# Kernel tuning notes

Hardware: AMD Instinct MI355X
Metric: run time of the kernel (lower is better)

Reference implementation:

```python
import jax, jax.numpy as jnp
import numpy as np

N_SEGMENT = 8   # frames per clip (init arg n_segment)
P = 4           # patch_size (init arg)
EPS = 1e-5      # torch F.layer_norm default eps


def setup_inputs() -> dict:
    key = jax.random.key(0)
    # (b*t, c, h, w) = (16*8, 256, 28, 28)
    x = jax.random.normal(key, (128, 256, 28, 28), dtype=jnp.float32)
    return {"x": x}


def _layer_norm(x):
    # F.layer_norm over last dim, no affine params
    m = jnp.mean(x, axis=-1, keepdims=True)
    v = jnp.var(x, axis=-1, keepdims=True)
    return (x - m) * jax.lax.rsqrt(v + EPS)


def _self_attention(x):
    # q = k = v = x; scores = softmax(q k^T / sqrt(E)); out = scores @ v
    e = x.shape[-1]
    scores = jnp.einsum('bqe,bke->bqk', x, x) * (1.0 / float(np.sqrt(e)))
    scores = jax.nn.softmax(scores, axis=-1)
    return jnp.einsum('bqk,bke->bqe', scores, x)


def reference(x):
    t, p = N_SEGMENT, P
    bt, c, h, w = x.shape
    b = bt // t
    ph, pw = h // p, w // p
    e = p * p * c  # patch embedding dim = 4096

    # rearrange '(b t) c (ph p1) (pw p2) -> (b ph pw) t (p1 p2 c)'
    y = x.reshape(b, t, c, ph, p, pw, p)
    y = y.transpose(0, 3, 5, 1, 4, 6, 2).reshape(b * ph * pw, t, e)

    # temporal: layernorm + shift-left-diff + self-attention + residual
    xn = _layer_norm(y)
    xn = jnp.concatenate([xn[:, 1:], jnp.zeros_like(xn[:, :1])], axis=1) - xn
    y = _self_attention(xn) + y

    # rearrange '(b ph pw) t e -> (b t) (ph pw) e'
    y = y.reshape(b, ph, pw, t, e).transpose(0, 3, 1, 2, 4).reshape(b * t, ph * pw, e)

    # spatial: layernorm + self-attention + residual
    xn = _layer_norm(y)
    y = _self_attention(xn) + y

    # rearrange '(b t) (ph pw) (p1 p2 c) -> (b t) c (ph p1) (pw p2)'
    y = y.reshape(b, t, ph, pw, p, p, c)
    y = y.transpose(0, 1, 6, 2, 4, 3, 5).reshape(bt, c, h, w)
    return y
```

## Files before the change

kernel.cpp:

```cpp
#include <hip/hip_runtime.h>


#define IDX36(a,b) ((((a)*8)+(b))-((((a)*((a)+1)))/2))

typedef __attribute__((ext_vector_type(8)))  short bf16x8;
typedef __attribute__((ext_vector_type(16))) float f32x16;

__device__ __forceinline__ float wsum64(float v){
  #pragma unroll
  for (int off=32; off; off>>=1) v += __shfl_xor(v, off);
  return v;
}
__device__ __forceinline__ float wsum32(float v){
  #pragma unroll
  for (int off=16; off; off>>=1) v += __shfl_xor(v, off);
  return v;
}
__device__ __forceinline__ unsigned int rne_bf16(float f){
  unsigned int b = __float_as_uint(f);
  return (b + 0x7FFFu + ((b>>16)&1u)) >> 16;
}

__global__ __launch_bounds__(256) void k_t1(const float* __restrict__ x, float* __restrict__ wsG){
  const int bx = blockIdx.x;
  const int b = bx / 112;
  const int ph = (bx % 112) / 16;
  const int slice = bx & 15;
  const int c0 = slice * 16;
  const int tid = threadIdx.x;

  __shared__ float lds[8*16*116];
  const float4* x4 = reinterpret_cast<const float4*>(x);

  #pragma unroll
  for (int t=0;t<8;t++){
    const int base = ((b*8+t)*256 + c0)*196 + ph*28;
    {
      const int f = tid, c = f/28, m = f%28;
      *reinterpret_cast<float4*>(&lds[(t*16+c)*116 + m*4]) = x4[base + c*196 + m];
    }
    if (tid < 192){
      const int f = 256+tid, c = f/28, m = f%28;
      *reinterpret_cast<float4*>(&lds[(t*16+c)*116 + m*4]) = x4[base + c*196 + m];
    }
  }
  __syncthreads();

  const int pw   = tid >> 5;
  const int slot = tid & 31;
  const int c    = slot >> 1;
  const int p1b  = (slot & 1) * 2;

  float v[8][8];
  #pragma unroll
  for (int t=0;t<8;t++){
    const float* p = &lds[(t*16+c)*116 + p1b*28 + pw*4];
    const float4 a  = *reinterpret_cast<const float4*>(p);
    const float4 b2 = *reinterpret_cast<const float4*>(p + 28);
    v[t][0]=a.x;  v[t][1]=a.y;  v[t][2]=a.z;  v[t][3]=a.w;
    v[t][4]=b2.x; v[t][5]=b2.y; v[t][6]=b2.z; v[t][7]=b2.w;
  }

  float Au[36], sm[8];
  #pragma unroll
  for (int a2=0;a2<8;a2++){
    float s0 = 0.f;
    #pragma unroll
    for (int e=0;e<8;e++) s0 += v[a2][e];
    sm[a2] = s0;
    #pragma unroll
    for (int b2=a2;b2<8;b2++){
      float s = 0.f;
      #pragma unroll
      for (int e=0;e<8;e++) s += v[a2][e]*v[b2][e];
      Au[IDX36(a2,b2)] = s;
    }
  }
  #pragma unroll
  for (int i=0;i<36;i++) Au[i] = wsum32(Au[i]);
  #pragma unroll
  for (int t=0;t<8;t++) sm[t] = wsum32(sm[t]);

  if (slot == 0 && pw < 7){
    const int base = ((b*49 + ph*7 + pw)*16 + slice)*44;
    #pragma unroll
    for (int i=0;i<36;i++) wsG[base+i] = Au[i];
    #pragma unroll
    for (int t=0;t<8;t++)  wsG[base+36+t] = sm[t];
  }
}

__global__ __launch_bounds__(64) void k_t2(const float* __restrict__ wsG, float* __restrict__ wsWt){
  const int seq = blockIdx.x;
  const int lane = threadIdx.x;
  __shared__ float red[44];
  if (lane < 44){
    float a = 0.f;
    #pragma unroll
    for (int s=0;s<16;s++) a += wsG[(seq*16+s)*44 + lane];
    red[lane] = a;
  }
  __syncthreads();
  if (lane < 8){
    const int i = lane;
    float Ar[36], mean[8], rstd[8];
    #pragma unroll
    for (int k=0;k<36;k++) Ar[k] = red[k];
    #pragma unroll
    for (int t=0;t<8;t++){
      const float sv = red[36+t];
      mean[t] = sv * (1.f/4096.f);
      const float var = Ar[IDX36(t,t)] * (1.f/4096.f) - mean[t]*mean[t];
      rstd[t] = rsqrtf(var + 1e-5f);
    }
    #define GV(a,b) ((((a)<8)&&((b)<8)) ? (rstd[(a)]*rstd[(b)]*(Ar[((a)<=(b))?IDX36((a),(b)):IDX36((b),(a))] - 4096.f*mean[(a)]*mean[(b)])) : 0.f)
    float l[8]; float mx = -1e30f;
    #pragma unroll
    for (int j=0;j<8;j++){
      const float sij = GV(i+1,j+1) - GV(i+1,j) - GV(i,j+1) + GV(i,j);
      l[j] = sij * (1.f/64.f);
      mx = fmaxf(mx, l[j]);
    }
    float ss = 0.f;
    #pragma unroll
    for (int j=0;j<8;j++){ l[j] = __expf(l[j]-mx); ss += l[j]; }
    const float inv = 1.f/ss;
    float cc = 0.f;
    #pragma unroll
    for (int k2=0;k2<8;k2++){
      const float q = (((k2>=1)? l[k2-1] : 0.f) - l[k2]) * inv;
      const float wv2 = q * rstd[k2];
      wsWt[seq*72 + i*8 + k2] = wv2;
      cc -= wv2 * mean[k2];
    }
    wsWt[seq*72 + 64 + i] = cc;
    #undef GV
  }
}

__global__ __launch_bounds__(256) void k_t3(const float* __restrict__ x, const float* __restrict__ wsWt,
                                            float* __restrict__ y1){
  const int bx = blockIdx.x;
  const int b = bx / 112;
  const int ph = (bx % 112) / 16;
  const int slice = bx & 15;
  const int c0 = slice * 16;
  const int tid = threadIdx.x;

  __shared__ float Wl[7][72];
  for (int idx=tid; idx<504; idx+=256)
    Wl[idx/72][idx%72] = wsWt[(b*49 + ph*7 + idx/72)*72 + idx%72];
  __syncthreads();

  const float4* x4 = reinterpret_cast<const float4*>(x);
  float4* y4 = reinterpret_cast<float4*>(y1);

  #pragma unroll
  for (int fi=0; fi<2; fi++){
    const int f = fi*256 + tid;
    if (f < 448){
      const int c = f/28, m = f%28, pw = m%7, p1 = m/7;
      float4 v[8];
      #pragma unroll
      for (int t=0;t<8;t++) v[t] = x4[((b*8+t)*256 + c0+c)*196 + ph*28 + m];
      const float* W = Wl[pw];
      const int pp = ph*7 + pw;
      #pragma unroll
      for (int i=0;i<8;i++){
        const float ci = W[64+i];
        float4 o;
        o.x = v[i].x + ci; o.y = v[i].y + ci; o.z = v[i].z + ci; o.w = v[i].w + ci;
        #pragma unroll
        for (int j=0;j<8;j++){
          const float w = W[i*8+j];
          o.x += w*v[j].x; o.y += w*v[j].y; o.z += w*v[j].z; o.w += w*v[j].w;
        }
        y4[((b*8+i)*49 + pp)*1024 + (c0+c)*4 + p1] = o;
      }
    }
  }
}

__global__ __launch_bounds__(256,2) void k_s1(const float* __restrict__ y1, float* __restrict__ wsA){
  const int bt = blockIdx.x >> 2;
  const int slice = blockIdx.x & 3;
  const int tid = threadIdx.x;
  const int wave = tid >> 6, lane = tid & 63;

  __shared__ unsigned short Ah[64*136];
  __shared__ unsigned short Al[64*136];
  __shared__ float red[64*52];

  for (int i=tid; i<64*52; i+=256) red[i] = 0.f;

  f32x16 acc00, acc01, acc11;
  #pragma unroll
  for (int i=0;i<16;i++){ acc00[i]=0.f; acc01[i]=0.f; acc11[i]=0.f; }

  const float4* yb4 = reinterpret_cast<const float4*>(y1 + bt*49*4096 + slice*1024);
  const int rgrp = tid >> 5;
  const int col4 = tid & 31;
  const int r0 = lane & 31;
  const int koff = (lane >> 5) * 8;

#define ISSUE_CH(pf, ch) { \
  _Pragma("unroll") \
  for (int i=0;i<7;i++) pf[i] = yb4[(i*8 + rgrp)*1024 + (ch)*32 + col4]; }

#define CW_CH(pf) { \
  _Pragma("unroll") \
  for (int i=0;i<8;i++){ \
    unsigned int h01,h23,l01,l23; \
    if (i==7){ h01=0u; h23=0u; l01=0u; l23=0u; } \
    else { \
      const float4 v = pf[i]; \
      const unsigned int u0=__float_as_uint(v.x), u1=__float_as_uint(v.y); \
      const unsigned int u2=__float_as_uint(v.z), u3=__float_as_uint(v.w); \
      const float l0 = v.x-__uint_as_float(u0&0xFFFF0000u); \
      const float l1 = v.y-__uint_as_float(u1&0xFFFF0000u); \
      const float l2 = v.z-__uint_as_float(u2&0xFFFF0000u); \
      const float l3 = v.w-__uint_as_float(u3&0xFFFF0000u); \
      h01 = (u0>>16)|(u1&0xFFFF0000u); h23 = (u2>>16)|(u3&0xFFFF0000u); \
      l01 = rne_bf16(l0)|(rne_bf16(l1)<<16); l23 = rne_bf16(l2)|(rne_bf16(l3)<<16); \
      if (i==6){ \
        const bool valid = (rgrp==0); const bool ones = (rgrp==1); \
        h01 = valid ? h01 : (ones ? 0x3F803F80u : 0u); \
        h23 = valid ? h23 : (ones ? 0x3F803F80u : 0u); \
        l01 = valid ? l01 : 0u; l23 = valid ? l23 : 0u; \
      } \
    } \
    const int wb = (i*8+rgrp)*136 + col4*4; \
    *reinterpret_cast<uint2*>(&Ah[wb]) = make_uint2(h01,h23); \
    *reinterpret_cast<uint2*>(&Al[wb]) = make_uint2(l01,l23); \
  } }

#define MFMA_CH() { \
  _Pragma("unroll") \
  for (int kk=0;kk<2;kk++){ \
    const int kw = (wave + kk*4)*16; \
    const bf16x8 f0h = *reinterpret_cast<const bf16x8*>(&Ah[ r0     *136 + kw + koff]); \
    const bf16x8 f0l = *reinterpret_cast<const bf16x8*>(&Al[ r0     *136 + kw + koff]); \
    const bf16x8 f1h = *reinterpret_cast<const bf16x8*>(&Ah[(32+r0)*136 + kw + koff]); \
    const bf16x8 f1l = *reinterpret_cast<const bf16x8*>(&Al[(32+r0)*136 + kw + koff]); \
    acc00 = __builtin_amdgcn_mfma_f32_32x32x16_bf16(f0h, f0h, acc00, 0,0,0); \
    acc00 = __builtin_amdgcn_mfma_f32_32x32x16_bf16(f0h, f0l, acc00, 0,0,0); \
    acc00 = __builtin_amdgcn_mfma_f32_32x32x16_bf16(f0l, f0h, acc00, 0,0,0); \
    acc01 = __builtin_amdgcn_mfma_f32_32x32x16_bf16(f0h, f1h, acc01, 0,0,0); \
    acc01 = __builtin_amdgcn_mfma_f32_32x32x16_bf16(f0h, f1l, acc01, 0,0,0); \
    acc01 = __builtin_amdgcn_mfma_f32_32x32x16_bf16(f0l, f1h, acc01, 0,0,0); \
    acc11 = __builtin_amdgcn_mfma_f32_32x32x16_bf16(f1h, f1h, acc11, 0,0,0); \
    acc11 = __builtin_amdgcn_mfma_f32_32x32x16_bf16(f1h, f1l, acc11, 0,0,0); \
    acc11 = __builtin_amdgcn_mfma_f32_32x32x16_bf16(f1l, f1h, acc11, 0,0,0); \
  } }

  float4 pfA[7], pfB[7];
  ISSUE_CH(pfA, 0);
  #pragma unroll
  for (int ch=0; ch<8; ch+=2){
    if (ch+1<8) ISSUE_CH(pfB, ch+1);
    __syncthreads();
    CW_CH(pfA);
    __syncthreads();
    MFMA_CH();
    if (ch+2<8) ISSUE_CH(pfA, ch+2);
    __syncthreads();
    CW_CH(pfB);
    __syncthreads();
    MFMA_CH();
  }
  __syncthreads();

  const int ccol = lane & 31;
  const int rbase = 4*(lane>>5);
  #pragma unroll
  for (int q2=0;q2<16;q2++){
    const int rr = (q2&3) + 8*(q2>>2) + rbase;
    atomicAdd(&red[ rr    *52 + ccol     ], acc00[q2]);
    atomicAdd(&red[ rr    *52 + 32 + ccol], acc01[q2]);
    atomicAdd(&red[(rr+32)*52 + 32 + ccol], acc11[q2]);
  }
  __syncthreads();
  float* wp = wsA + blockIdx.x * 2500;
  for (int idx=tid; idx<2500; idx+=256){
    const int i2 = idx/50, j2 = idx%50;
    wp[idx] = (i2>=32 && j2<32) ? red[j2*52+i2] : red[i2*52+j2];
  }
#undef ISSUE_CH
#undef CW_CH
#undef MFMA_CH
}

__global__ __launch_bounds__(256) void k_s2(const float* __restrict__ wsA, float* __restrict__ wsWT, float* __restrict__ wsC){
  const int bt = blockIdx.x;
  const int tid = threadIdx.x;
  __shared__ float A[2500];
  __shared__ float m[49], r[49];
  for (int idx=tid; idx<2548; idx+=256) wsWT[bt*2548+idx] = 0.f;
  for (int idx=tid; idx<2500; idx+=256){
    float v = 0.f;
    #pragma unroll
    for (int sl=0; sl<4; sl++) v += wsA[(bt*4+sl)*2500 + idx];
    A[idx] = v;
  }
  __syncthreads();
  if (tid < 49){
    const float mm = A[49*50+tid] * (1.f/4096.f);
    const float var = A[tid*50+tid] * (1.f/4096.f) - mm*mm;
    m[tid]=mm; r[tid]=rsqrtf(var+1e-5f);
  }
  __syncthreads();
  const int wv = tid>>6, lane = tid&63;
  for (int i=wv; i<49; i+=4){
    const float ri = r[i], mi = m[i];
    float rv=0.f, mv=0.f, L=-1e30f;
    if (lane < 49){
      rv = r[lane]; mv = m[lane];
      L = ri*rv*(A[i*50+lane] - 4096.f*mi*mv) * (1.f/64.f);
    }
    float mx = L;
    #pragma unroll
    for (int off=32; off; off>>=1) mx = fmaxf(mx, __shfl_xor(mx, off));
    const float p = (lane<49) ? __expf(L-mx) : 0.f;
    const float ss = wsum64(p);
    const float Wv = (p/ss)*rv;
    if (lane < 49) wsWT[bt*2548 + lane*52 + i] = Wv + ((lane==i) ? 1.f : 0.f);
    const float cp = wsum64(-Wv*mv);
    if (lane == 0) wsC[bt*49+i] = cp;
  }
}

__global__ __launch_bounds__(256,2) void k_s3(const float* __restrict__ y1, const float* __restrict__ wsWT,
                                              const float* __restrict__ wsC, float* __restrict__ out){
  const int bt = blockIdx.x >> 2;
  const int chunk = blockIdx.x & 3;
  const int tid = threadIdx.x;
  const int wave = tid >> 6, lane = tid & 63;

  __shared__ unsigned short Wh[64*68], Wlo[64*68];
  __shared__ unsigned short Yh[4][32*68], Ylo[4][32*68];

  for (int idx=tid; idx<64*64; idx+=256){
    const int i = idx>>6, j = idx&63;
    float v = 0.f;
    if (i < 49){
      if (j < 49)       v = wsWT[bt*2548 + j*52 + i];
      else if (j == 49) v = wsC[bt*49 + i];
    }
    const unsigned int u = __float_as_uint(v);
    const float lo = v - __uint_as_float(u & 0xFFFF0000u);
    Wh [i*68+j] = (unsigned short)(u>>16);
    Wlo[i*68+j] = (unsigned short)rne_bf16(lo);
  }
  unsigned short* yh = &Yh[wave][0];
  unsigned short* yl = &Ylo[wave][0];
  for (int idx=lane; idx<32*16; idx+=64){
    const int e = idx>>4, jj = idx&15;
    if (jj > 0){
      yh[e*68 + 48 + jj] = (jj==1) ? 0x3F80 : 0;
      yl[e*68 + 48 + jj] = 0;
    }
  }
  __syncthreads();

  const int r0 = lane & 31;
  const int koff = (lane >> 5) * 8;
  bf16x8 A0h[4], A0l[4], A1h[4], A1l[4];
  #pragma unroll
  for (int kk=0;kk<4;kk++){
    const int off = kk*16 + koff;
    A0h[kk] = *reinterpret_cast<const bf16x8*>(&Wh [ r0     *68 + off]);
    A0l[kk] = *reinterpret_cast<const bf16x8*>(&Wlo[ r0     *68 + off]);
    A1h[kk] = *reinterpret_cast<const bf16x8*>(&Wh [(32+r0)*68 + off]);
    A1l[kk] = *reinterpret_cast<const bf16x8*>(&Wlo[(32+r0)*68 + off]);
  }

  const float4* yb4 = reinterpret_cast<const float4*>(y1 + bt*200704 + chunk*1024);
  float* ob_base = out + bt*200704;

#define S3_LOAD(pf, t) { \
  _Pragma("unroll") \
  for (int p=0;p<7;p++){ \
    const int idx = p*64 + lane; const int j = idx>>3, e4 = idx&7; \
    pf[p] = make_float4(0.f,0.f,0.f,0.f); \
    if (j < 49) pf[p] = yb4[j*1024 + ((t)*4+wave)*8 + e4]; \
  } }

#define S3_WRITE(pf) { \
  _Pragma("unroll") \
  for (int p=0;p<7;p++){ \
    const int idx = p*64 + lane; const int j = idx>>3, e4 = idx&7; \
    if (j < 49){ \
      const float vv[4] = {pf[p].x, pf[p].y, pf[p].z, pf[p].w}; \
      _Pragma("unroll") \
      for (int s=0;s<4;s++){ \
        const unsigned int u = __float_as_uint(vv[s]); \
        const float lo = vv[s] - __uint_as_float(u & 0xFFFF0000u); \
        yh[(e4*4+s)*68 + j] = (unsigned short)(u>>16); \
        yl[(e4*4+s)*68 + j] = (unsigned short)rne_bf16(lo); \
      } \
    } \
  } }

  float4 pf[7];
  S3_LOAD(pf, 0);
  S3_WRITE(pf);

  #pragma unroll
  for (int t=0;t<8;t++){
    if (t < 7) S3_LOAD(pf, t+1);

    f32x16 acc0, acc1;
    #pragma unroll
    for (int i=0;i<16;i++){ acc0[i]=0.f; acc1[i]=0.f; }

    #pragma unroll
    for (int kk=0;kk<4;kk++){
      const int off = kk*16 + koff;
      const bf16x8 Bh = *reinterpret_cast<const bf16x8*>(&yh[r0*68 + off]);
      const bf16x8 Bl = *reinterpret_cast<const bf16x8*>(&yl[r0*68 + off]);
      acc0 = __builtin_amdgcn_mfma_f32_32x32x16_bf16(A0h[kk], Bh, acc0, 0,0,0);
      acc0 = __builtin_amdgcn_mfma_f32_32x32x16_bf16(A0h[kk], Bl, acc0, 0,0,0);
      acc0 = __builtin_amdgcn_mfma_f32_32x32x16_bf16(A0l[kk], Bh, acc0, 0,0,0);
      acc1 = __builtin_amdgcn_mfma_f32_32x32x16_bf16(A1h[kk], Bh, acc1, 0,0,0);
      acc1 = __builtin_amdgcn_mfma_f32_32x32x16_bf16(A1h[kk], Bl, acc1, 0,0,0);
      acc1 = __builtin_amdgcn_mfma_f32_32x32x16_bf16(A1l[kk], Bh, acc1, 0,0,0);
    }

    {
      const int ecol = chunk*1024 + (t*4+wave)*32 + r0;
      const int c  = ecol >> 4;
      const int p1 = (ecol >> 2) & 3;
      const int p2 = ecol & 3;
      float* ob = ob_base + c*784 + p1*28 + p2;
      const int rbase = 4*(lane>>5);
      #pragma unroll
      for (int q=0;q<16;q++){
        const int i0 = (q&3) + 8*(q>>2) + rbase;
        ob[(i0/7)*112 + (i0%7)*4] = acc0[q];
        const int i1 = 32 + i0;
        if (i1 < 49) ob[(i1/7)*112 + (i1%7)*4] = acc1[q];
      }
    }

    if (t < 7) S3_WRITE(pf);
  }
#undef S3_LOAD
#undef S3_WRITE
}

extern "C" void kernel_launch(void* const* d_in, const int* in_sizes, int n_in,
                              void* d_out, int out_size, void* d_ws, size_t ws_size,
                              hipStream_t stream) {
  const float* x = (const float*)d_in[0];
  float* out = (float*)d_out;
  float* ws  = (float*)d_ws;
  float* y1   = ws;
  float* wsA  = y1 + 25690112;
  float* wsWT = wsA + 512*2500;
  float* wsC  = wsWT + 128*2548;
  float* wsG  = wsA;
  float* wsWt = wsA + 551936;
  hipLaunchKernelGGL(k_t1, dim3(1792), dim3(256), 0, stream, x, wsG);
  hipLaunchKernelGGL(k_t2, dim3(784),  dim3(64),  0, stream, wsG, wsWt);
  hipLaunchKernelGGL(k_t3, dim3(1792), dim3(256), 0, stream, x, wsWt, y1);
  hipLaunchKernelGGL(k_s1, dim3(512),  dim3(256), 0, stream, y1, wsA);
  hipLaunchKernelGGL(k_s2, dim3(128),  dim3(256), 0, stream, wsA, wsWT, wsC);
  hipLaunchKernelGGL(k_s3, dim3(512),  dim3(256), 0, stream, y1, wsWT, wsC, out);
}
```

Measured before the change: 197.7 us.

## Store intermediate as pre-split bf16 hi/lo planes and use bf16-only Gram in s1

k_t3 now writes the intermediate y1 as two bf16 planes (high and residual low) instead of fp32, moving the split work out of the consumers. k_s1 now reads only the high plane and computes the spatial Gram matrix with a single bf16 MFMA per tile instead of three split-precision products. Dropping the low-plane buffer frees LDS, so occupancy is raised to 3 blocks. k_s3 loads the pre-split planes directly. Intermediate traffic stays the same size, but the spatial attention scores lose the hi/lo correction terms, which risks accuracy.

```diff
diff --git a/kernel.cpp b/kernel.cpp
--- a/kernel.cpp
+++ b/kernel.cpp
@@ -139,7 +139,7 @@
 }
 
 __global__ __launch_bounds__(256) void k_t3(const float* __restrict__ x, const float* __restrict__ wsWt,
-                                            float* __restrict__ y1){
+                                            unsigned short* __restrict__ y1u){
   const int bx = blockIdx.x;
   const int b = bx / 112;
   const int ph = (bx % 112) / 16;
@@ -153,7 +153,6 @@
   __syncthreads();
 
   const float4* x4 = reinterpret_cast<const float4*>(x);
-  float4* y4 = reinterpret_cast<float4*>(y1);
 
   #pragma unroll
   for (int fi=0; fi<2; fi++){
@@ -175,98 +174,80 @@
           const float w = W[i*8+j];
           o.x += w*v[j].x; o.y += w*v[j].y; o.z += w*v[j].z; o.w += w*v[j].w;
         }
-        y4[((b*8+i)*49 + pp)*1024 + (c0+c)*4 + p1] = o;
+        const unsigned int h0=rne_bf16(o.x), h1=rne_bf16(o.y), h2=rne_bf16(o.z), h3=rne_bf16(o.w);
+        const unsigned int l0=rne_bf16(o.x-__uint_as_float(h0<<16));
+        const unsigned int l1=rne_bf16(o.y-__uint_as_float(h1<<16));
+        const unsigned int l2=rne_bf16(o.z-__uint_as_float(h2<<16));
+        const unsigned int l3=rne_bf16(o.w-__uint_as_float(h3<<16));
+        const size_t ybase = (size_t)((b*8+i)*49 + pp)*8192 + (c0+c)*16 + p1*4;
+        *reinterpret_cast<uint2*>(&y1u[ybase])        = make_uint2(h0|(h1<<16), h2|(h3<<16));
+        *reinterpret_cast<uint2*>(&y1u[ybase + 4096]) = make_uint2(l0|(l1<<16), l2|(l3<<16));
       }
     }
   }
 }
 
-__global__ __launch_bounds__(256,2) void k_s1(const float* __restrict__ y1, float* __restrict__ wsA){
+__global__ __launch_bounds__(256,3) void k_s1(const unsigned short* __restrict__ y1u, float* __restrict__ wsA){
   const int bt = blockIdx.x >> 2;
   const int slice = blockIdx.x & 3;
   const int tid = threadIdx.x;
   const int wave = tid >> 6, lane = tid & 63;
 
   __shared__ unsigned short Ah[64*136];
-  __shared__ unsigned short Al[64*136];
   __shared__ float red[64*52];
-
   for (int i=tid; i<64*52; i+=256) red[i] = 0.f;
 
+  for (int idx=tid; idx<15*128; idx+=256){
+    const int rr = 49 + idx/128, cc = idx%128;
+    Ah[rr*136 + cc] = (rr==49) ? (unsigned short)0x3F80 : (unsigned short)0;
+  }
+
   f32x16 acc00, acc01, acc11;
   #pragma unroll
   for (int i=0;i<16;i++){ acc00[i]=0.f; acc01[i]=0.f; acc11[i]=0.f; }
 
-  const float4* yb4 = reinterpret_cast<const float4*>(y1 + bt*49*4096 + slice*1024);
-  const int rgrp = tid >> 5;
-  const int col4 = tid & 31;
   const int r0 = lane & 31;
   const int koff = (lane >> 5) * 8;
-
-#define ISSUE_CH(pf, ch) { \
+  const int lrow = tid >> 4;
+  const int lq   = tid & 15;
+
+#define ISSUE(pf, ch) { \
   _Pragma("unroll") \
-  for (int i=0;i<7;i++) pf[i] = yb4[(i*8 + rgrp)*1024 + (ch)*32 + col4]; }
-
-#define CW_CH(pf) { \
+  for (int p=0;p<4;p++){ \
+    const int row = p*16 + lrow; \
+    pf[p] = make_uint4(0u,0u,0u,0u); \
+    if (row < 49) pf[p] = *reinterpret_cast<const uint4*>(&y1u[(size_t)(bt*49+row)*8192 + slice*1024 + (ch)*128 + lq*8]); } }
+
+#define CW(pf) { \
   _Pragma("unroll") \
-  for (int i=0;i<8;i++){ \
-    unsigned int h01,h23,l01,l23; \
-    if (i==7){ h01=0u; h23=0u; l01=0u; l23=0u; } \
-    else { \
-      const float4 v = pf[i]; \
-      const unsigned int u0=__float_as_uint(v.x), u1=__float_as_uint(v.y); \
-      const unsigned int u2=__float_as_uint(v.z), u3=__float_as_uint(v.w); \
-      const float l0 = v.x-__uint_as_float(u0&0xFFFF0000u); \
-      const float l1 = v.y-__uint_as_float(u1&0xFFFF0000u); \
-      const float l2 = v.z-__uint_as_float(u2&0xFFFF0000u); \
-      const float l3 = v.w-__uint_as_float(u3&0xFFFF0000u); \
-      h01 = (u0>>16)|(u1&0xFFFF0000u); h23 = (u2>>16)|(u3&0xFFFF0000u); \
-      l01 = rne_bf16(l0)|(rne_bf16(l1)<<16); l23 = rne_bf16(l2)|(rne_bf16(l3)<<16); \
-      if (i==6){ \
-        const bool valid = (rgrp==0); const bool ones = (rgrp==1); \
-        h01 = valid ? h01 : (ones ? 0x3F803F80u : 0u); \
-        h23 = valid ? h23 : (ones ? 0x3F803F80u : 0u); \
-        l01 = valid ? l01 : 0u; l23 = valid ? l23 : 0u; \
-      } \
-    } \
-    const int wb = (i*8+rgrp)*136 + col4*4; \
-    *reinterpret_cast<uint2*>(&Ah[wb]) = make_uint2(h01,h23); \
-    *reinterpret_cast<uint2*>(&Al[wb]) = make_uint2(l01,l23); \
-  } }
-
-#define MFMA_CH() { \
+  for (int p=0;p<4;p++){ \
+    const int row = p*16 + lrow; \
+    if (row < 49) *reinterpret_cast<uint4*>(&Ah[row*136 + lq*8]) = pf[p]; } }
+
+#define MF() { \
   _Pragma("unroll") \
   for (int kk=0;kk<2;kk++){ \
     const int kw = (wave + kk*4)*16; \
-    const bf16x8 f0h = *reinterpret_cast<const bf16x8*>(&Ah[ r0     *136 + kw + koff]); \
-    const bf16x8 f0l = *reinterpret_cast<const bf16x8*>(&Al[ r0     *136 + kw + koff]); \
-    const bf16x8 f1h = *reinterpret_cast<const bf16x8*>(&Ah[(32+r0)*136 + kw + koff]); \
-    const bf16x8 f1l = *reinterpret_cast<const bf16x8*>(&Al[(32+r0)*136 + kw + koff]); \
-    acc00 = __builtin_amdgcn_mfma_f32_32x32x16_bf16(f0h, f0h, acc00, 0,0,0); \
-    acc00 = __builtin_amdgcn_mfma_f32_32x32x16_bf16(f0h, f0l, acc00, 0,0,0); \
-    acc00 = __builtin_amdgcn_mfma_f32_32x32x16_bf16(f0l, f0h, acc00, 0,0,0); \
-    acc01 = __builtin_amdgcn_mfma_f32_32x32x16_bf16(f0h, f1h, acc01, 0,0,0); \
-    acc01 = __builtin_amdgcn_mfma_f32_32x32x16_bf16(f0h, f1l, acc01, 0,0,0); \
-    acc01 = __builtin_amdgcn_mfma_f32_32x32x16_bf16(f0l, f1h, acc01, 0,0,0); \
-    acc11 = __builtin_amdgcn_mfma_f32_32x32x16_bf16(f1h, f1h, acc11, 0,0,0); \
-    acc11 = __builtin_amdgcn_mfma_f32_32x32x16_bf16(f1h, f1l, acc11, 0,0,0); \
-    acc11 = __builtin_amdgcn_mfma_f32_32x32x16_bf16(f1l, f1h, acc11, 0,0,0); \
-  } }
-
-  float4 pfA[7], pfB[7];
-  ISSUE_CH(pfA, 0);
+    const bf16x8 f0 = *reinterpret_cast<const bf16x8*>(&Ah[ r0     *136 + kw + koff]); \
+    const bf16x8 f1 = *reinterpret_cast<const bf16x8*>(&Ah[(32+r0)*136 + kw + koff]); \
+    acc00 = __builtin_amdgcn_mfma_f32_32x32x16_bf16(f0, f0, acc00, 0,0,0); \
+    acc01 = __builtin_amdgcn_mfma_f32_32x32x16_bf16(f0, f1, acc01, 0,0,0); \
+    acc11 = __builtin_amdgcn_mfma_f32_32x32x16_bf16(f1, f1, acc11, 0,0,0); } }
+
+  uint4 pfA[4], pfB[4];
+  ISSUE(pfA, 0);
   #pragma unroll
   for (int ch=0; ch<8; ch+=2){
-    if (ch+1<8) ISSUE_CH(pfB, ch+1);
+    if (ch+1<8) ISSUE(pfB, ch+1);
     __syncthreads();
-    CW_CH(pfA);
+    CW(pfA);
     __syncthreads();
-    MFMA_CH();
-    if (ch+2<8) ISSUE_CH(pfA, ch+2);
+    MF();
+    if (ch+2<8) ISSUE(pfA, ch+2);
     __syncthreads();
-    CW_CH(pfB);
+    CW(pfB);
     __syncthreads();
-    MFMA_CH();
+    MF();
   }
   __syncthreads();
 
@@ -285,9 +266,9 @@
     const int i2 = idx/50, j2 = idx%50;
     wp[idx] = (i2>=32 && j2<32) ? red[j2*52+i2] : red[i2*52+j2];
   }
-#undef ISSUE_CH
-#undef CW_CH
-#undef MFMA_CH
+#undef ISSUE
+#undef CW
+#undef MF
 }
 
 __global__ __launch_bounds__(256) void k_s2(const float* __restrict__ wsA, float* __restrict__ wsWT, float* __restrict__ wsC){
@@ -329,7 +310,7 @@
   }
 }
 
-__global__ __launch_bounds__(256,2) void k_s3(const float* __restrict__ y1, const float* __restrict__ wsWT,
+__global__ __launch_bounds__(256,2) void k_s3(const unsigned short* __restrict__ y1u, const float* __restrict__ wsWT,
                                               const float* __restrict__ wsC, float* __restrict__ out){
   const int bt = blockIdx.x >> 2;
   const int chunk = blockIdx.x & 3;
@@ -374,34 +355,31 @@
     A1l[kk] = *reinterpret_cast<const bf16x8*>(&Wlo[(32+r0)*68 + off]);
   }
 
-  const float4* yb4 = reinterpret_cast<const float4*>(y1 + bt*200704 + chunk*1024);
+  const unsigned short* ybu = y1u + (size_t)bt*49*8192;
   float* ob_base = out + bt*200704;
 
 #define S3_LOAD(pf, t) { \
+  const int ecol0 = chunk*1024 + ((t)*4+wave)*32; \
   _Pragma("unroll") \
   for (int p=0;p<7;p++){ \
-    const int idx = p*64 + lane; const int j = idx>>3, e4 = idx&7; \
-    pf[p] = make_float4(0.f,0.f,0.f,0.f); \
-    if (j < 49) pf[p] = yb4[j*1024 + ((t)*4+wave)*8 + e4]; \
-  } }
+    const int idx = p*64 + lane; const int j = idx>>3; const int sub = idx&7; \
+    pf[p] = make_uint4(0u,0u,0u,0u); \
+    if (j < 49) pf[p] = *reinterpret_cast<const uint4*>(&ybu[(size_t)j*8192 + (sub>>2)*4096 + ecol0 + (sub&3)*8]); } }
 
 #define S3_WRITE(pf) { \
   _Pragma("unroll") \
   for (int p=0;p<7;p++){ \
-    const int idx = p*64 + lane; const int j = idx>>3, e4 = idx&7; \
+    const int idx = p*64 + lane; const int j = idx>>3; const int sub = idx&7; \
     if (j < 49){ \
-      const float vv[4] = {pf[p].x, pf[p].y, pf[p].z, pf[p].w}; \
+      unsigned short* dst = (sub>>2) ? yl : yh; \
+      const int e0 = (sub&3)*8; \
+      const unsigned int uu[4] = {pf[p].x, pf[p].y, pf[p].z, pf[p].w}; \
       _Pragma("unroll") \
       for (int s=0;s<4;s++){ \
-        const unsigned int u = __float_as_uint(vv[s]); \
-        const float lo = vv[s] - __uint_as_float(u & 0xFFFF0000u); \
-        yh[(e4*4+s)*68 + j] = (unsigned short)(u>>16); \
-        yl[(e4*4+s)*68 + j] = (unsigned short)rne_bf16(lo); \
-      } \
-    } \
-  } }
-
-  float4 pf[7];
+        dst[(e0 + s*2    )*68 + j] = (unsigned short)(uu[s] & 0xFFFFu); \
+        dst[(e0 + s*2 + 1)*68 + j] = (unsigned short)(uu[s] >> 16); } } } }
+
+  uint4 pf[7];
   S3_LOAD(pf, 0);
   S3_WRITE(pf);
 
@@ -454,16 +432,16 @@
   const float* x = (const float*)d_in[0];
   float* out = (float*)d_out;
   float* ws  = (float*)d_ws;
-  float* y1   = ws;
-  float* wsA  = y1 + 25690112;
+  unsigned short* y1u = (unsigned short*)ws;
+  float* wsA  = ws + 25690112;
   float* wsWT = wsA + 512*2500;
   float* wsC  = wsWT + 128*2548;
   float* wsG  = wsA;
   float* wsWt = wsA + 551936;
   hipLaunchKernelGGL(k_t1, dim3(1792), dim3(256), 0, stream, x, wsG);
   hipLaunchKernelGGL(k_t2, dim3(784),  dim3(64),  0, stream, wsG, wsWt);
-  hipLaunchKernelGGL(k_t3, dim3(1792), dim3(256), 0, stream, x, wsWt, y1);
-  hipLaunchKernelGGL(k_s1, dim3(512),  dim3(256), 0, stream, y1, wsA);
+  hipLaunchKernelGGL(k_t3, dim3(1792), dim3(256), 0, stream, x, wsWt, y1u);
+  hipLaunchKernelGGL(k_s1, dim3(512),  dim3(256), 0, stream, y1u, wsA);
   hipLaunchKernelGGL(k_s2, dim3(128),  dim3(256), 0, stream, wsA, wsWT, wsC);
-  hipLaunchKernelGGL(k_s3, dim3(512),  dim3(256), 0, stream, y1, wsWT, wsC, out);
-}
+  hipLaunchKernelGGL(k_s3, dim3(512),  dim3(256), 0, stream, y1u, wsWT, wsC, out);
+}
```

Measured after the change: 199.9 us. No clear change (+1.1%).
